# Optimization experiments

Measured on AMD Instinct MI355X. Metric: run time of the kernel, lower is better.

The kernel has to match this reference:

```python
import jax, jax.numpy as jnp
import numpy as np

B, M, C_IN, H, W = 8, 64, 2048, 16, 16
IMG = 512          # image size in pixels (feature stride 32)
OUT = 7            # ROIAlign output size
SCALE = 1.0 / 32.0
SR = 2             # samples per bin; equals ceil(roi_extent/7) for the generated boxes (sampling_ratio=0 behavior)
C2 = C_IN // 2     # 1024
D_ROI, D_BOX = 1024, 256
D_PAIR = 2 * (D_ROI + D_BOX)   # 2560
D_G = D_PAIR // 2              # 1280


def setup_inputs() -> dict:
    key = jax.random.key(0)
    ks = jax.random.split(key, 12)
    s = 0.02
    im_feat = jax.random.normal(ks[0], (B, C_IN, H, W), jnp.float32)
    # XYXY boxes; sizes in (230,440)px so scaled roi extent is in (7,14] -> adaptive sampling ratio == 2
    xy1 = jax.random.uniform(ks[1], (B, M, 2), jnp.float32, 0.0, 60.0)
    wh = jax.random.uniform(ks[2], (B, M, 2), jnp.float32, 230.0, 440.0)
    boxes = jnp.concatenate([xy1, xy1 + wh], -1)
    normalized_boxes = boxes / IMG
    params = dict(
        proj_w=jax.random.normal(ks[3], (C2, C_IN), jnp.float32) * s, proj_b=jnp.zeros((C2,), jnp.float32),
        conv_w=jax.random.normal(ks[4], (256, C2, 3, 3), jnp.float32) * s, conv_b=jnp.zeros((256,), jnp.float32),
        bn_g=jnp.ones((256,), jnp.float32), bn_b=jnp.zeros((256,), jnp.float32),
        bn_m=jnp.zeros((256,), jnp.float32), bn_v=jnp.ones((256,), jnp.float32),
        fc_w=jax.random.normal(ks[5], (D_ROI, 256 * OUT * OUT), jnp.float32) * s, fc_b=jnp.zeros((D_ROI,), jnp.float32),
        ln1_g=jnp.ones((D_ROI,), jnp.float32), ln1_b=jnp.zeros((D_ROI,), jnp.float32),
        box_w=jax.random.normal(ks[6], (D_BOX, 4), jnp.float32) * s, box_b=jnp.zeros((D_BOX,), jnp.float32),
        ln2_g=jnp.ones((D_BOX,), jnp.float32), ln2_b=jnp.zeros((D_BOX,), jnp.float32),
        g1_w=jax.random.normal(ks[7], (D_G, D_PAIR), jnp.float32) * s, g1_b=jnp.zeros((D_G,), jnp.float32),
        g2_w=jax.random.normal(ks[8], (D_G, D_G), jnp.float32) * s, g2_b=jnp.zeros((D_G,), jnp.float32),
        g3_w=jax.random.normal(ks[9], (D_G, D_G), jnp.float32) * s, g3_b=jnp.zeros((D_G,), jnp.float32),
    )
    return dict(im_feat=im_feat, boxes=boxes, normalized_boxes=normalized_boxes, **params)


def _layer_norm(x, g, b, eps=1e-5):
    mu = x.mean(-1, keepdims=True)
    var = ((x - mu) ** 2).mean(-1, keepdims=True)
    return (x - mu) * jax.lax.rsqrt(var + eps) * g + b


def _roi_align(feat, rois, bidx):
    # feat [B,C,Hf,Wf]; rois [N,4] XYXY image coords; bidx [N] int. ROIAlignV2 (aligned=True), 2x2 samples/bin.
    Hf, Wf = feat.shape[2], feat.shape[3]
    x1 = rois[:, 0] * SCALE - 0.5
    y1 = rois[:, 1] * SCALE - 0.5
    bw = (rois[:, 2] - rois[:, 0]) * SCALE / OUT
    bh = (rois[:, 3] - rois[:, 1]) * SCALE / OUT
    ii = (jnp.arange(OUT * SR, dtype=jnp.float32) + 0.5) / SR  # sample offsets in bin units
    xs = x1[:, None] + bw[:, None] * ii[None, :]               # [N, OUT*SR]
    ys = y1[:, None] + bh[:, None] * ii[None, :]

    def interp1(v, size):
        valid = (v >= -1.0) & (v <= size)
        v = jnp.clip(v, 0.0, None)
        lo = jnp.floor(v).astype(jnp.int32)
        over = lo >= size - 1
        lo = jnp.where(over, size - 1, lo)
        v = jnp.where(over, lo.astype(v.dtype), v)
        hi = jnp.where(over, lo, lo + 1)
        return lo, hi, v - lo, valid

    def bilin(b, ys_, xs_):
        img = feat[b]  # [C,Hf,Wf]
        yl, yh, wy, vy = interp1(ys_, Hf)
        xl, xh, wx, vx = interp1(xs_, Wf)
        g = lambda yi, xi: img[:, yi][:, :, xi]  # [C,S,S]
        val = (g(yl, xl) * (1 - wy)[None, :, None] * (1 - wx)[None, None, :]
               + g(yl, xh) * (1 - wy)[None, :, None] * wx[None, None, :]
               + g(yh, xl) * wy[None, :, None] * (1 - wx)[None, None, :]
               + g(yh, xh) * wy[None, :, None] * wx[None, None, :])
        mask = (vy[:, None] & vx[None, :]).astype(val.dtype)
        return val * mask

    vals = jax.vmap(bilin)(bidx, ys, xs)  # [N,C,OUT*SR,OUT*SR]
    N, C = vals.shape[0], vals.shape[1]
    return vals.reshape(N, C, OUT, SR, OUT, SR).mean((3, 5))  # avg over samples per bin


def reference(im_feat, boxes, normalized_boxes, proj_w, proj_b, conv_w, conv_b, bn_g, bn_b, bn_m, bn_v,
              fc_w, fc_b, ln1_g, ln1_b, box_w, box_b, ln2_g, ln2_b, g1_w, g1_b, g2_w, g2_b, g3_w, g3_b):
    # 1x1 conv projection
    x = jnp.einsum('bchw,oc->bohw', im_feat, proj_w) + proj_b[None, :, None, None]
    rois = boxes.reshape(B * M, 4)
    bidx = jnp.repeat(jnp.arange(B), M)
    r = _roi_align(x, rois, bidx)  # [BM, C2, 7, 7]
    # roi_processor: conv3x3 -> BN(eval) -> ReLU -> flatten -> Linear -> ReLU
    r = jax.lax.conv_general_dilated(r, conv_w, (1, 1), 'SAME',
                                     dimension_numbers=('NCHW', 'OIHW', 'NCHW')) + conv_b[None, :, None, None]
    r = (r - bn_m[None, :, None, None]) * jax.lax.rsqrt(bn_v + 1e-5)[None, :, None, None] \
        * bn_g[None, :, None, None] + bn_b[None, :, None, None]
    r = jax.nn.relu(r)
    r = jax.nn.relu(r.reshape(B * M, -1) @ fc_w.T + fc_b)
    r = _layer_norm(r, ln1_g, ln1_b)                       # [BM, 1024]
    nb = normalized_boxes.reshape(B * M, 4) * 2.0 - 1.0
    bf = _layer_norm(nb @ box_w.T + box_b, ln2_g, ln2_b)   # [BM, 256]
    feats = jnp.concatenate([r, bf], -1).reshape(B, M, D_ROI + D_BOX)

    def rel(xm):  # relation network over one image's M rois
        xi = jnp.broadcast_to(xm[None, :, :], (M, M, D_ROI + D_BOX))  # xi[a,b]=x[b]
        xj = jnp.broadcast_to(xm[:, None, :], (M, M, D_ROI + D_BOX))  # xj[a,b]=x[a]
        p = jnp.concatenate([xi, xj], -1).reshape(M * M, D_PAIR)
        h = jax.nn.relu(p @ g1_w.T + g1_b)
        h = jax.nn.relu(h @ g2_w.T + g2_b)
        h = jax.nn.relu(h @ g3_w.T + g3_b)
        return h.sum(0)

    return jax.vmap(rel)(feats)  # [B, 1280]
```

## Files before the change

### kernel.cpp

```cpp
#include <hip/hip_runtime.h>
#include <hip/hip_bf16.h>

typedef __attribute__((ext_vector_type(8))) short short8;
typedef __attribute__((ext_vector_type(4))) float floatx4;
typedef unsigned short u16;

#define GLDS16(gp, lp) __builtin_amdgcn_global_load_lds(                        \
    (const __attribute__((address_space(1))) void*)(gp),                        \
    (__attribute__((address_space(3))) void*)(lp), 16, 0, 0)

__device__ inline u16 f2bf(float f) {
    unsigned u = __float_as_uint(f);
    unsigned r = (u + 0x7fffu + ((u >> 16) & 1u)) >> 16;
    return (u16)r;
}

__device__ inline void block_reduce2(float& s, float& ss) {
    #pragma unroll
    for (int o = 32; o > 0; o >>= 1) {
        s  += __shfl_down(s, o);
        ss += __shfl_down(ss, o);
    }
    __shared__ float red[8];
    const int t = threadIdx.x;
    if ((t & 63) == 0) { red[t >> 6] = s; red[4 + (t >> 6)] = ss; }
    __syncthreads();
    s  = red[0] + red[1] + red[2] + red[3];
    ss = red[4] + red[5] + red[6] + red[7];
}

template<int AMODE, int EPI, int CMODE>
__global__ __launch_bounds__(256)
void gemm_bf16(const u16* __restrict__ A, const u16* __restrict__ B,
               const float* __restrict__ P1, const float* __restrict__ P2,
               void* __restrict__ Cv,
               int M, int N, int Kc, int lda, int ldb, int ldc)
{
    __shared__ short As[128 * 32];
    __shared__ short Bs[128 * 32];

    const int t  = threadIdx.x;
    const int w  = t >> 6, l = t & 63;
    const int wr = w >> 1, wc = w & 1;
    const int l16 = l & 15, lr = l >> 4;

    const int nwg = gridDim.x * gridDim.y;
    const int bid = blockIdx.y * gridDim.x + blockIdx.x;
    const int cpx = nwg >> 3;
    const int sw  = (bid & 7) * cpx + (bid >> 3);
    const int n0 = (sw % gridDim.x) * 128;
    const int m0 = (sw / gridDim.x) * 128;
    const int kbase = blockIdx.z * Kc;

    const int srow  = w * 16 + (l >> 2);
    const int skoff = (l & 3) * 8;

    const u16* aRow0 = nullptr; const u16* aRow1 = nullptr;
    size_t aSp0 = 0, aSp1 = 0;
    if (AMODE == 0) {
        aRow0 = A + (size_t)(m0 + srow) * lda + kbase + skoff;
        aRow1 = A + (size_t)(m0 + 64 + srow) * lda + kbase + skoff;
    } else {
        const int r0 = m0 + srow, r1 = r0 + 64;
        const int roi0 = r0 / 49, sp0 = r0 - roi0 * 49;
        const int roi1 = r1 / 49, sp1 = r1 - roi1 * 49;
        aSp0 = ((size_t)roi0 * 81 + (sp0 / 7) * 9 + (sp0 % 7)) * 1024 + skoff;
        aSp1 = ((size_t)roi1 * 81 + (sp1 / 7) * 9 + (sp1 % 7)) * 1024 + skoff;
    }
    const u16* bRow0 = B + (size_t)(n0 + srow) * ldb + kbase + skoff;
    const u16* bRow1 = B + (size_t)(n0 + 64 + srow) * ldb + kbase + skoff;

    short* lA0 = As + w * 512;
    short* lA1 = As + 2048 + w * 512;
    short* lB0 = Bs + w * 512;
    short* lB1 = Bs + 2048 + w * 512;

    floatx4 acc[4][4] = {};

    for (int k0 = 0; k0 < Kc; k0 += 32) {
        if (AMODE == 0) {
            GLDS16(aRow0 + k0, lA0);
            GLDS16(aRow1 + k0, lA1);
        } else {
            const int kk  = kbase + k0;
            const int tap = kk >> 10;
            const size_t off = (size_t)((tap / 3) * 9 + (tap % 3)) * 1024 + (kk & 1023);
            GLDS16(A + aSp0 + off, lA0);
            GLDS16(A + aSp1 + off, lA1);
        }
        GLDS16(bRow0 + k0, lB0);
        GLDS16(bRow1 + k0, lB1);
        __syncthreads();

        short8 af[4], bfr[4];
        #pragma unroll
        for (int i = 0; i < 4; ++i)
            af[i] = *reinterpret_cast<const short8*>(&As[(wr * 64 + i * 16 + l16) * 32 + lr * 8]);
        #pragma unroll
        for (int j = 0; j < 4; ++j)
            bfr[j] = *reinterpret_cast<const short8*>(&Bs[(wc * 64 + j * 16 + l16) * 32 + lr * 8]);
        #pragma unroll
        for (int i = 0; i < 4; ++i)
            #pragma unroll
            for (int j = 0; j < 4; ++j)
                acc[i][j] = __builtin_amdgcn_mfma_f32_16x16x32_bf16(af[i], bfr[j], acc[i][j], 0, 0, 0);
        __syncthreads();
    }

    const int mBase = m0 + wr * 64;
    const int nBase = n0 + wc * 64;

    if (CMODE == 2) {
        __shared__ float red2[2][128];
        float csum[4];
        #pragma unroll
        for (int j = 0; j < 4; ++j) {
            const int n = nBase + j * 16 + l16;
            const float b1 = P1[n];
            float s = 0.f;
            #pragma unroll
            for (int i = 0; i < 4; ++i)
                #pragma unroll
                for (int r = 0; r < 4; ++r)
                    s += fmaxf(acc[i][j][r] + b1, 0.f);
            s += __shfl_xor(s, 16);
            s += __shfl_xor(s, 32);
            csum[j] = s;
        }
        if (l < 16) {
            #pragma unroll
            for (int j = 0; j < 4; ++j)
                red2[wr][wc * 64 + j * 16 + l16] = csum[j];
        }
        __syncthreads();
        float* C = (float*)Cv + (size_t)(m0 >> 12) * ldc;
        if (t < 128) atomicAdd(&C[n0 + t], red2[0][t] + red2[1][t]);
        return;
    }

    #pragma unroll
    for (int i = 0; i < 4; ++i) {
        #pragma unroll
        for (int j = 0; j < 4; ++j) {
            const int n = nBase + j * 16 + l16;
            const float b1 = (EPI >= 1) ? P1[n] : 0.f;
            const float b2 = (EPI == 3) ? P2[n] : 0.f;
            #pragma unroll
            for (int r = 0; r < 4; ++r) {
                float v = acc[i][j][r];
                if (EPI == 1)      v += b1;
                else if (EPI == 2) v = fmaxf(v + b1, 0.f);
                else if (EPI == 3) v = fmaxf(v * b1 + b2, 0.f);
                const int m = mBase + i * 16 + lr * 4 + r;
                if (CMODE == 0)      ((float*)Cv)[(size_t)m * ldc + n] = v;
                else if (CMODE == 4) ((u16*)Cv)[(size_t)m * ldc + n] = f2bf(v);
                else if (CMODE == 3) atomicAdd(&((float*)Cv)[(size_t)m * ldc + n], v);
                else if (CMODE == 1) {
                    const int roi = m / 49, sp = m - roi * 49;
                    ((u16*)Cv)[(size_t)roi * 12544 + n * 49 + sp] = f2bf(v);
                }
            }
        }
    }
}

__global__ __launch_bounds__(256)
void transpose_proj(const float* __restrict__ in, u16* __restrict__ out)
{
    __shared__ float tile[64][65];
    const int b = blockIdx.z;
    const int c0 = blockIdx.y * 64;
    const int h0 = blockIdx.x * 64;
    const int t = threadIdx.x;
    const float* src = in + ((size_t)b * 2048 + c0) * 256 + h0;
    #pragma unroll
    for (int p = 0; p < 16; ++p) {
        const int idx = p * 256 + t;
        const int r = idx >> 6, c = idx & 63;
        tile[r][c] = src[(size_t)r * 256 + c];
    }
    __syncthreads();
    u16* dst = out + ((size_t)b * 256 + h0) * 2048 + c0;
    #pragma unroll
    for (int p = 0; p < 16; ++p) {
        const int idx = p * 256 + t;
        const int r = idx >> 6, c = idx & 63;
        dst[(size_t)r * 2048 + c] = f2bf(tile[c][r]);
    }
}

__global__ __launch_bounds__(256)
void zero_halo(u16* __restrict__ r_pad)
{
    const int blk = blockIdx.x;
    const int roi = blk >> 5, h = blk & 31;
    int p;
    if (h < 9)       p = h;
    else if (h < 18) p = 72 + (h - 9);
    else { const int r = (h - 18) >> 1, s = (h - 18) & 1; p = (r + 1) * 9 + s * 8; }
    uint2* o = reinterpret_cast<uint2*>(r_pad + ((size_t)roi * 81 + p) * 1024);
    o[threadIdx.x] = make_uint2(0u, 0u);
}

__global__ __launch_bounds__(256)
void roialign_kernel(const float* __restrict__ x_cl, const float* __restrict__ boxes,
                     u16* __restrict__ r_pad)
{
    const int blk = blockIdx.x;
    const int n = blk / 49, bin = blk % 49;
    const int py = bin / 7, px = bin % 7;
    const int b = n >> 6;
    const float* roi = boxes + n * 4;
    const float x1 = roi[0] * (1.f/32.f) - 0.5f;
    const float y1 = roi[1] * (1.f/32.f) - 0.5f;
    const float bw = (roi[2] - roi[0]) * (1.f/32.f) * (1.0f / 7.0f);
    const float bh = (roi[3] - roi[1]) * (1.f/32.f) * (1.0f / 7.0f);
    const int t = threadIdx.x;

    float acc[4] = {0.f, 0.f, 0.f, 0.f};
    #pragma unroll
    for (int sy = 0; sy < 2; ++sy) {
        #pragma unroll
        for (int sx = 0; sx < 2; ++sx) {
            const float yv = y1 + bh * ((float)(py * 2 + sy) + 0.5f) * 0.5f;
            const float xv = x1 + bw * ((float)(px * 2 + sx) + 0.5f) * 0.5f;
            const bool vy = (yv >= -1.0f) && (yv <= 16.0f);
            const bool vx = (xv >= -1.0f) && (xv <= 16.0f);
            if (!(vy && vx)) continue;
            float yc = fmaxf(yv, 0.f);
            int yl = (int)floorf(yc);
            int yh; if (yl >= 15) { yl = 15; yc = 15.f; yh = 15; } else yh = yl + 1;
            const float wy = yc - (float)yl;
            float xc = fmaxf(xv, 0.f);
            int xl = (int)floorf(xc);
            int xh; if (xl >= 15) { xl = 15; xc = 15.f; xh = 15; } else xh = xl + 1;
            const float wx = xc - (float)xl;

            const float w00 = (1.f - wy) * (1.f - wx), w01 = (1.f - wy) * wx;
            const float w10 = wy * (1.f - wx),         w11 = wy * wx;
            const float* p00 = x_cl + ((size_t)b * 256 + yl * 16 + xl) * 1024;
            const float* p01 = x_cl + ((size_t)b * 256 + yl * 16 + xh) * 1024;
            const float* p10 = x_cl + ((size_t)b * 256 + yh * 16 + xl) * 1024;
            const float* p11 = x_cl + ((size_t)b * 256 + yh * 16 + xh) * 1024;
            #pragma unroll
            for (int cc = 0; cc < 4; ++cc) {
                const int c = t + cc * 256;
                acc[cc] += w00 * p00[c] + w01 * p01[c] + w10 * p10[c] + w11 * p11[c];
            }
        }
    }
    u16* o = r_pad + ((size_t)n * 81 + (py + 1) * 9 + (px + 1)) * 1024;
    #pragma unroll
    for (int cc = 0; cc < 4; ++cc) o[t + cc * 256] = f2bf(acc[cc] * 0.25f);
}

__global__ __launch_bounds__(256)
void pack_conv(const float* __restrict__ conv_w, const float* __restrict__ conv_b,
               const float* __restrict__ bn_g, const float* __restrict__ bn_b,
               const float* __restrict__ bn_m, const float* __restrict__ bn_v,
               u16* __restrict__ wpack, float* __restrict__ scale, float* __restrict__ shift)
{
    const long idx = (long)blockIdx.x * 256 + threadIdx.x;
    if (idx < 2359296L) {
        const int oc = (int)(idx / 9216), k = (int)(idx % 9216);
        const int tap = k >> 10, ic = k & 1023;
        wpack[idx] = f2bf(conv_w[(long)oc * 9216 + ic * 9 + tap]);
    }
    if (idx < 256) {
        const float s = bn_g[idx] * rsqrtf(bn_v[idx] + 1e-5f);
        scale[idx] = s;
        shift[idx] = (conv_b[idx] - bn_m[idx]) * s + bn_b[idx];
    }
}

__global__ __launch_bounds__(256)
void cvt_bf16(const float* __restrict__ in, u16* __restrict__ out, int n4)
{
    const int i = blockIdx.x * 256 + threadIdx.x;
    if (i < n4) {
        const float4 v = reinterpret_cast<const float4*>(in)[i];
        ushort4 o; o.x = f2bf(v.x); o.y = f2bf(v.y); o.z = f2bf(v.z); o.w = f2bf(v.w);
        reinterpret_cast<ushort4*>(out)[i] = o;
    }
}

__global__ __launch_bounds__(256)
void pack_g1(const float* __restrict__ g1w, u16* __restrict__ out)
{
    const int j = blockIdx.x * 256 + threadIdx.x;
    if (j >= 2560 * 320) return;
    const int np = j / 320, k4 = (j - np * 320) * 4;
    const int srow = (np < 1280) ? np : np - 1280;
    const int soff = (np < 1280) ? 0 : 1280;
    const float4 v = *reinterpret_cast<const float4*>(&g1w[(size_t)srow * 2560 + soff + k4]);
    ushort4 o; o.x = f2bf(v.x); o.y = f2bf(v.y); o.z = f2bf(v.z); o.w = f2bf(v.w);
    *reinterpret_cast<ushort4*>(&out[(size_t)np * 1280 + k4]) = o;
}

__global__ __launch_bounds__(256)
void ln1_kernel(const float* __restrict__ in, const float* __restrict__ fb,
                const float* __restrict__ g, const float* __restrict__ b,
                u16* __restrict__ feats)
{
    const int n = blockIdx.x, t = threadIdx.x;
    float4 v = *reinterpret_cast<const float4*>(in + (size_t)n * 1024 + t * 4);
    const float4 bb = *reinterpret_cast<const float4*>(fb + t * 4);
    v.x = fmaxf(v.x + bb.x, 0.f); v.y = fmaxf(v.y + bb.y, 0.f);
    v.z = fmaxf(v.z + bb.z, 0.f); v.w = fmaxf(v.w + bb.w, 0.f);
    float s  = v.x + v.y + v.z + v.w;
    float ss = v.x*v.x + v.y*v.y + v.z*v.z + v.w*v.w;
    block_reduce2(s, ss);
    const float mu  = s * (1.f / 1024.f);
    const float var = ss * (1.f / 1024.f) - mu * mu;
    const float r   = rsqrtf(var + 1e-5f);
    const float4 gp = *reinterpret_cast<const float4*>(g + t * 4);
    const float4 bp = *reinterpret_cast<const float4*>(b + t * 4);
    ushort4 o;
    o.x = f2bf((v.x - mu) * r * gp.x + bp.x);
    o.y = f2bf((v.y - mu) * r * gp.y + bp.y);
    o.z = f2bf((v.z - mu) * r * gp.z + bp.z);
    o.w = f2bf((v.w - mu) * r * gp.w + bp.w);
    *reinterpret_cast<ushort4*>(feats + (size_t)n * 1280 + t * 4) = o;
}

__global__ __launch_bounds__(256)
void box_kernel(const float* __restrict__ nb, const float* __restrict__ bw,
                const float* __restrict__ bb, const float* __restrict__ g,
                const float* __restrict__ be, u16* __restrict__ feats)
{
    const int n = blockIdx.x, j = threadIdx.x;
    const float4 q = *reinterpret_cast<const float4*>(nb + n * 4);
    const float4 w = *reinterpret_cast<const float4*>(bw + j * 4);
    const float v = (q.x * 2.f - 1.f) * w.x + (q.y * 2.f - 1.f) * w.y
                  + (q.z * 2.f - 1.f) * w.z + (q.w * 2.f - 1.f) * w.w + bb[j];
    float s = v, ss = v * v;
    block_reduce2(s, ss);
    const float mu  = s * (1.f / 256.f);
    const float var = ss * (1.f / 256.f) - mu * mu;
    feats[(size_t)n * 1280 + 1024 + j] = f2bf((v - mu) * rsqrtf(var + 1e-5f) * g[j] + be[j]);
}

__global__ __launch_bounds__(256)
void pair_kernel(const float* __restrict__ UV, const float* __restrict__ g1b,
                 u16* __restrict__ h1, int imgbase)
{
    const int pidx = blockIdx.y;
    const int img = imgbase + (pidx >> 12);
    const int a = (pidx >> 6) & 63, b = pidx & 63;
    const int col = blockIdx.x * 256 + threadIdx.x;
    const float v = UV[(size_t)(img * 64 + b) * 2560 + col]
                  + UV[(size_t)(img * 64 + a) * 2560 + 1280 + col] + g1b[col];
    h1[(size_t)pidx * 1280 + col] = f2bf(fmaxf(v, 0.f));
}

__global__ void zero_f32(float* __restrict__ p, int n) {
    const int i = blockIdx.x * 256 + threadIdx.x;
    if (i < n) p[i] = 0.f;
}

extern "C" void kernel_launch(void* const* d_in, const int* in_sizes, int n_in,
                              void* d_out, int out_size, void* d_ws, size_t ws_size,
                              hipStream_t stream)
{
    const float* im_feat = (const float*)d_in[0];
    const float* boxes   = (const float*)d_in[1];
    const float* nboxes  = (const float*)d_in[2];
    const float* proj_w  = (const float*)d_in[3];
    const float* proj_b  = (const float*)d_in[4];
    const float* conv_w  = (const float*)d_in[5];
    const float* conv_b  = (const float*)d_in[6];
    const float* bn_g    = (const float*)d_in[7];
    const float* bn_b    = (const float*)d_in[8];
    const float* bn_m    = (const float*)d_in[9];
    const float* bn_v    = (const float*)d_in[10];
    const float* fc_w    = (const float*)d_in[11];
    const float* fc_b    = (const float*)d_in[12];
    const float* ln1_g   = (const float*)d_in[13];
    const float* ln1_b   = (const float*)d_in[14];
    const float* box_w   = (const float*)d_in[15];
    const float* box_b   = (const float*)d_in[16];
    const float* ln2_g   = (const float*)d_in[17];
    const float* ln2_b   = (const float*)d_in[18];
    const float* g1_w    = (const float*)d_in[19];
    const float* g1_b    = (const float*)d_in[20];
    const float* g2_w    = (const float*)d_in[21];
    const float* g2_b    = (const float*)d_in[22];
    const float* g3_w    = (const float*)d_in[23];
    const float* g3_b    = (const float*)d_in[24];
    float* out = (float*)d_out;
    (void)in_sizes; (void)n_in; (void)out_size; (void)ws_size;

    char* base = (char*)d_ws;
    size_t o = 0;
    auto carve = [&](size_t bytes) { char* p = base + o; o += (bytes + 15) & ~(size_t)15; return p; };
    float* x_cl    = (float*)carve(8388608);
    u16*   imT     = (u16*)  carve(8388608);
    u16*   convout = (u16*)  carve(12845056);
    float* fc_out  = (float*)carve(2097152);
    u16*   feats   = (u16*)  carve(1310720);
    float* UV      = (float*)carve(5242880);
    u16*   wpack   = (u16*)  carve(4718592);
    float* scale   = (float*)carve(1024);
    float* shift   = (float*)carve(1024);
    u16*   projwb  = (u16*)  carve(4194304);
    u16*   fcwb    = (u16*)  carve(25690112);
    u16*   g1wb    = (u16*)  carve(6553600);
    u16*   g2wb    = (u16*)  carve(3276800);
    u16*   g3wb    = (u16*)  carve(3276800);
    char*  big     = carve(84934656);
    u16*   r_pad   = (u16*)big;
    u16*   h1      = (u16*)big;
    u16*   h2      = (u16*)(big + 41943040);

    zero_f32<<<40, 256, 0, stream>>>(out, 10240);
    zero_f32<<<2048, 256, 0, stream>>>(fc_out, 524288);
    zero_f32<<<5120, 256, 0, stream>>>(UV, 1310720);

    cvt_bf16<<<2048, 256, 0, stream>>>(proj_w, projwb, 524288);
    cvt_bf16<<<12544, 256, 0, stream>>>(fc_w, fcwb, 3211264);
    cvt_bf16<<<1600, 256, 0, stream>>>(g2_w, g2wb, 409600);
    cvt_bf16<<<1600, 256, 0, stream>>>(g3_w, g3wb, 409600);
    pack_g1<<<3200, 256, 0, stream>>>(g1_w, g1wb);
    pack_conv<<<9216, 256, 0, stream>>>(conv_w, conv_b, bn_g, bn_b, bn_m, bn_v, wpack, scale, shift);

    transpose_proj<<<dim3(4, 32, 8), 256, 0, stream>>>(im_feat, imT);
    gemm_bf16<0, 1, 0><<<dim3(8, 16, 1), 256, 0, stream>>>(
        imT, projwb, proj_b, nullptr, x_cl, 2048, 1024, 2048, 2048, 2048, 1024);

    zero_halo<<<16384, 256, 0, stream>>>(r_pad);
    roialign_kernel<<<25088, 256, 0, stream>>>(x_cl, boxes, r_pad);

    gemm_bf16<2, 3, 1><<<dim3(2, 196, 1), 256, 0, stream>>>(
        r_pad, wpack, scale, shift, convout, 25088, 256, 9216, 0, 9216, 0);

    gemm_bf16<0, 0, 3><<<dim3(8, 4, 4), 256, 0, stream>>>(
        convout, fcwb, nullptr, nullptr, fc_out, 512, 1024, 3136, 12544, 12544, 1024);

    ln1_kernel<<<512, 256, 0, stream>>>(fc_out, fc_b, ln1_g, ln1_b, feats);
    box_kernel<<<512, 256, 0, stream>>>(nboxes, box_w, box_b, ln2_g, ln2_b, feats);

    gemm_bf16<0, 0, 3><<<dim3(20, 4, 2), 256, 0, stream>>>(
        feats, g1wb, nullptr, nullptr, UV, 512, 2560, 640, 1280, 1280, 2560);

    for (int h = 0; h < 2; ++h) {
        pair_kernel<<<dim3(5, 16384), 256, 0, stream>>>(UV, g1_b, h1, h * 4);
        gemm_bf16<0, 2, 4><<<dim3(10, 128, 1), 256, 0, stream>>>(
            h1, g2wb, g2_b, nullptr, h2, 16384, 1280, 1280, 1280, 1280, 1280);
        gemm_bf16<0, 2, 2><<<dim3(10, 128, 1), 256, 0, stream>>>(
            h2, g3wb, g3_b, nullptr, out + h * 4 * 1280, 16384, 1280, 1280, 1280, 1280, 1280);
    }
}
```

Baseline: 1.020 ms.

## Double-buffer LDS tiles in bf16 GEMM to overlap global loads with MFMA

Splits the LDS A/B tiles into two buffers and issues the global-to-LDS loads for the next K-slice before running the MFMAs on the current slice. This replaces the two __syncthreads per iteration with one vmcnt wait and barrier, so load latency can be hidden behind compute. It doubles LDS use per block to 32 KB, which may reduce occupancy, and adds a __syncthreads before the column-sum reduction in the epilogue.

```diff
diff --git a/kernel.cpp b/kernel.cpp
--- a/kernel.cpp
+++ b/kernel.cpp
@@ -36,8 +36,8 @@
                void* __restrict__ Cv,
                int M, int N, int Kc, int lda, int ldb, int ldc)
 {
-    __shared__ short As[128 * 32];
-    __shared__ short Bs[128 * 32];
+    __shared__ short As[2][4096];
+    __shared__ short Bs[2][4096];
 
     const int t  = threadIdx.x;
     const int w  = t >> 6, l = t & 63;
@@ -70,41 +70,52 @@
     const u16* bRow0 = B + (size_t)(n0 + srow) * ldb + kbase + skoff;
     const u16* bRow1 = B + (size_t)(n0 + 64 + srow) * ldb + kbase + skoff;
 
-    short* lA0 = As + w * 512;
-    short* lA1 = As + 2048 + w * 512;
-    short* lB0 = Bs + w * 512;
-    short* lB1 = Bs + 2048 + w * 512;
-
-    floatx4 acc[4][4] = {};
-
-    for (int k0 = 0; k0 < Kc; k0 += 32) {
+    auto stage = [&](int buf, int k0) {
         if (AMODE == 0) {
-            GLDS16(aRow0 + k0, lA0);
-            GLDS16(aRow1 + k0, lA1);
+            GLDS16(aRow0 + k0, As[buf] + w * 512);
+            GLDS16(aRow1 + k0, As[buf] + 2048 + w * 512);
         } else {
             const int kk  = kbase + k0;
             const int tap = kk >> 10;
             const size_t off = (size_t)((tap / 3) * 9 + (tap % 3)) * 1024 + (kk & 1023);
-            GLDS16(A + aSp0 + off, lA0);
-            GLDS16(A + aSp1 + off, lA1);
+            GLDS16(A + aSp0 + off, As[buf] + w * 512);
+            GLDS16(A + aSp1 + off, As[buf] + 2048 + w * 512);
         }
-        GLDS16(bRow0 + k0, lB0);
-        GLDS16(bRow1 + k0, lB1);
-        __syncthreads();
-
+        GLDS16(bRow0 + k0, Bs[buf] + w * 512);
+        GLDS16(bRow1 + k0, Bs[buf] + 2048 + w * 512);
+    };
+
+    floatx4 acc[4][4] = {};
+
+    stage(0, 0);
+    asm volatile("s_waitcnt vmcnt(0)" ::: "memory");
+    __builtin_amdgcn_s_barrier();
+    __builtin_amdgcn_sched_barrier(0);
+
+    int cur = 0;
+    for (int k0 = 0; k0 < Kc; k0 += 32) {
+        const int nxt = k0 + 32;
+        if (nxt < Kc) stage(cur ^ 1, nxt);
+
+        const short* as = As[cur];
+        const short* bs = Bs[cur];
         short8 af[4], bfr[4];
         #pragma unroll
         for (int i = 0; i < 4; ++i)
-            af[i] = *reinterpret_cast<const short8*>(&As[(wr * 64 + i * 16 + l16) * 32 + lr * 8]);
+            af[i] = *reinterpret_cast<const short8*>(&as[(wr * 64 + i * 16 + l16) * 32 + lr * 8]);
         #pragma unroll
         for (int j = 0; j < 4; ++j)
-            bfr[j] = *reinterpret_cast<const short8*>(&Bs[(wc * 64 + j * 16 + l16) * 32 + lr * 8]);
+            bfr[j] = *reinterpret_cast<const short8*>(&bs[(wc * 64 + j * 16 + l16) * 32 + lr * 8]);
         #pragma unroll
         for (int i = 0; i < 4; ++i)
             #pragma unroll
             for (int j = 0; j < 4; ++j)
                 acc[i][j] = __builtin_amdgcn_mfma_f32_16x16x32_bf16(af[i], bfr[j], acc[i][j], 0, 0, 0);
-        __syncthreads();
+
+        asm volatile("s_waitcnt vmcnt(0)" ::: "memory");
+        __builtin_amdgcn_s_barrier();
+        __builtin_amdgcn_sched_barrier(0);
+        cur ^= 1;
     }
 
     const int mBase = m0 + wr * 64;
@@ -127,6 +138,7 @@
             s += __shfl_xor(s, 32);
             csum[j] = s;
         }
+        __syncthreads();
         if (l < 16) {
             #pragma unroll
             for (int j = 0; j < 4; ++j)
```

After: 939.8 us. 7.9% less time.
